# Kernel optimization log

Measured on AMD Instinct MI355X. Metric: run time of the kernel, lower is better.

## Reference

```python
import jax, jax.numpy as jnp
import numpy as np


def silu(x):
    return x * jax.nn.sigmoid(x)


def setup_inputs() -> dict:
    key = jax.random.key(0)
    B, L, Din = 2, 512, 128
    E, K = 2, 4
    d = E * Din          # inner dim = 256
    N = d                # state size forced to hid_dim = expansion*input_dim
    R = d // 16          # dt low-rank = 16
    ks = jax.random.split(key, 12)
    s = 0.02
    rn = lambda k, sh: (jax.random.normal(k, sh, jnp.float32) * s)
    return {
        "x":      jax.random.normal(ks[0], (B, L, Din), jnp.float32),
        "W_in":   rn(ks[1], (Din, d)),  "b_in":  jnp.zeros((d,), jnp.float32),
        "W_res":  rn(ks[2], (Din, d)),  "b_res": jnp.zeros((d,), jnp.float32),
        "conv_w": rn(ks[3], (d, d, K)), "conv_b": jnp.zeros((d,), jnp.float32),
        "W_xdt":  rn(ks[4], (d, R)),
        "W_dt":   rn(ks[5], (R, d)),
        "b_dt":   jnp.full((d,), -4.6, jnp.float32),  # softplus -> dt ~ 0.01
        "W_B":    rn(ks[6], (d, N)),
        "W_C":    rn(ks[7], (d, N)),
        "A_log":  jnp.log(jnp.broadcast_to(jnp.arange(1, N + 1, dtype=jnp.float32), (d, N))),
        "D":      jnp.ones((d,), jnp.float32),
        "W_out":  rn(ks[8], (d, Din)), "b_out": jnp.zeros((Din,), jnp.float32),
    }


def reference(x, W_in, b_in, W_res, b_res, conv_w, conv_b,
              W_xdt, W_dt, b_dt, W_B, W_C, A_log, D, W_out, b_out):
    k = conv_w.shape[-1]
    # input projections
    xi = x @ W_in + b_in               # [B,L,d]
    x_res = silu(x @ W_res + b_res)    # [B,L,d] gate branch
    # causal full (groups=1) conv1d: padding k-1, truncated to length L
    c = jax.lax.conv_general_dilated(
        xi.transpose(0, 2, 1), conv_w, window_strides=(1,),
        padding=[(k - 1, 0)], dimension_numbers=("NCH", "OIH", "NCH"))
    u = silu((c + conv_b[None, :, None]).transpose(0, 2, 1))  # [B,L,d]
    # S6 selective scan
    delta = jax.nn.softplus((u @ W_xdt) @ W_dt + b_dt)  # [B,L,d]
    Bm = u @ W_B                                        # [B,L,N]
    Cm = u @ W_C                                        # [B,L,N]
    A = -jnp.exp(A_log)                                 # [d,N]

    def step(h, xs):
        u_t, d_t, B_t, C_t = xs                         # [B,d],[B,d],[B,N],[B,N]
        dA = jnp.exp(d_t[:, :, None] * A)               # [B,d,N]
        h = dA * h + (d_t * u_t)[:, :, None] * B_t[:, None, :]
        y = jnp.einsum("bdn,bn->bd", h, C_t)
        return h, y

    h0 = jnp.zeros((x.shape[0], A.shape[0], A.shape[1]), xi.dtype)
    xs = (u.transpose(1, 0, 2), delta.transpose(1, 0, 2),
          Bm.transpose(1, 0, 2), Cm.transpose(1, 0, 2))
    _, ys = jax.lax.scan(step, h0, xs)                  # ys: [L,B,d]
    y = ys.transpose(1, 0, 2) + u * D                   # skip connection D*u
    # residual gate + output projection (norm disabled)
    return (y + x_res) @ W_out + b_out
```

## Files before the change

### kernel.cpp

```cpp
#include <hip/hip_runtime.h>
#include <hip/hip_bf16.h>

#define kB   2
#define kL   512
#define kBL  1024
#define kDin 128
#define kD   256
#define kN   256
#define kR   16
#define kK   4
#define kS   8
#define kT   64

__device__ __forceinline__ float silu_f(float v) { return v / (1.f + __expf(-v)); }
__device__ __forceinline__ float softplus_f(float z) {
    return (z > 20.f) ? z : log1pf(__expf(z));
}
__device__ __forceinline__ float4 f4fma(float s, float4 w, float4 a) {
    a.x += s * w.x; a.y += s * w.y; a.z += s * w.z; a.w += s * w.w; return a;
}

__global__ void __launch_bounds__(256) pre_kernel(
        const float* __restrict__ x, const float* __restrict__ W_in,
        const float* __restrict__ b_in, const float* __restrict__ W_res,
        const float* __restrict__ b_res, const float* __restrict__ conv_w,
        float* __restrict__ wT, float* __restrict__ xi, float* __restrict__ xres) {
    __shared__ float tile[32][33];
    __shared__ float xs[2][kDin];
    __shared__ float red[128][9];
    int bid = blockIdx.x, tid = threadIdx.x;
    if (bid < 256) {
        int c0 = (bid & 31) * 32, r0 = (bid >> 5) * 32;
        int tx = tid & 31, ty = tid >> 5;
        #pragma unroll
        for (int j = 0; j < 32; j += 8)
            tile[ty + j][tx] = conv_w[(r0 + ty + j) * 1024 + c0 + tx];
        __syncthreads();
        #pragma unroll
        for (int j = 0; j < 32; j += 8)
            wT[(c0 + ty + j) * 256 + r0 + tx] = tile[tx][ty + j];
        return;
    }
    int bt0 = (bid - 256) * 2;
    xs[tid >> 7][tid & 127] = x[bt0 * kDin + tid];
    __syncthreads();
    int q = tid & 63, m = (tid >> 6) & 1, ks = tid >> 7;
    const float* W = m ? W_res : W_in;
    float4 a0 = {0,0,0,0}, a1 = {0,0,0,0};
    int i0 = ks * 64;
    #pragma unroll 4
    for (int i = i0; i < i0 + 64; i++) {
        float4 w = ((const float4*)(W + i * kD))[q];
        a0 = f4fma(xs[0][i], w, a0);
        a1 = f4fma(xs[1][i], w, a1);
    }
    if (ks) {
        float* rr = red[tid - 128];
        rr[0] = a0.x; rr[1] = a0.y; rr[2] = a0.z; rr[3] = a0.w;
        rr[4] = a1.x; rr[5] = a1.y; rr[6] = a1.z; rr[7] = a1.w;
    }
    __syncthreads();
    if (!ks) {
        const float* rr = red[tid];
        a0.x += rr[0]; a0.y += rr[1]; a0.z += rr[2]; a0.w += rr[3];
        a1.x += rr[4]; a1.y += rr[5]; a1.z += rr[6]; a1.w += rr[7];
        float4 bv = ((const float4*)(m ? b_res : b_in))[q];
        a0.x += bv.x; a0.y += bv.y; a0.z += bv.z; a0.w += bv.w;
        a1.x += bv.x; a1.y += bv.y; a1.z += bv.z; a1.w += bv.w;
        if (m) {
            float4 s0 = {silu_f(a0.x), silu_f(a0.y), silu_f(a0.z), silu_f(a0.w)};
            float4 s1 = {silu_f(a1.x), silu_f(a1.y), silu_f(a1.z), silu_f(a1.w)};
            ((float4*)(xres + (bt0 + 0) * kD))[q] = s0;
            ((float4*)(xres + (bt0 + 1) * kD))[q] = s1;
        } else {
            ((float4*)(xi + (bt0 + 0) * kD))[q] = a0;
            ((float4*)(xi + (bt0 + 1) * kD))[q] = a1;
        }
    }
}

__global__ void __launch_bounds__(512) conv_fwd(
        const float* __restrict__ xi, const float* __restrict__ wT,
        const float* __restrict__ conv_b, float* __restrict__ u) {
    __shared__ float xs[7][kD];
    __shared__ float red[7][64][17];
    int bid = blockIdx.x, tid = threadIdx.x;
    int b = bid >> 7, t0 = (bid & 127) * 4;
    for (int idx = tid; idx < 7 * kD; idx += 512) {
        int j = idx >> 8, i = idx & 255;
        int t = t0 - 3 + j;
        xs[j][i] = (t >= 0) ? xi[(b * kL + t) * kD + i] : 0.f;
    }
    __syncthreads();
    int q = tid & 63, ks = tid >> 6;
    float4 a[4] = {{0,0,0,0},{0,0,0,0},{0,0,0,0},{0,0,0,0}};
    int ik0 = ks * 128;
    #pragma unroll 4
    for (int ik = ik0; ik < ik0 + 128; ik++) {
        float4 w = ((const float4*)(wT + ik * kD))[q];
        int ii = ik >> 2, k = ik & 3;
        #pragma unroll
        for (int r = 0; r < 4; r++) a[r] = f4fma(xs[k + r][ii], w, a[r]);
    }
    if (ks) {
        float* rr = red[ks - 1][q];
        #pragma unroll
        for (int r = 0; r < 4; r++) {
            rr[4*r+0] = a[r].x; rr[4*r+1] = a[r].y;
            rr[4*r+2] = a[r].z; rr[4*r+3] = a[r].w;
        }
    }
    __syncthreads();
    if (!ks) {
        #pragma unroll
        for (int p = 0; p < 7; p++) {
            const float* rr = red[p][q];
            #pragma unroll
            for (int r = 0; r < 4; r++) {
                a[r].x += rr[4*r+0]; a[r].y += rr[4*r+1];
                a[r].z += rr[4*r+2]; a[r].w += rr[4*r+3];
            }
        }
        float4 cb = ((const float4*)conv_b)[q];
        #pragma unroll
        for (int r = 0; r < 4; r++) {
            float4 v = {silu_f(a[r].x + cb.x), silu_f(a[r].y + cb.y),
                        silu_f(a[r].z + cb.z), silu_f(a[r].w + cb.w)};
            ((float4*)(u + (b * kL + t0 + r) * kD))[q] = v;
        }
    }
}

__global__ void __launch_bounds__(256) proj_bcd(
        const float* __restrict__ u, const float* __restrict__ W_xdt,
        const float* __restrict__ W_dt, const float* __restrict__ b_dt,
        const float* __restrict__ W_B, const float* __restrict__ W_C,
        float* __restrict__ delta, float* __restrict__ Bm, float* __restrict__ Cm) {
    __shared__ float us[2][kD];
    __shared__ float tpart[128];
    __shared__ float ts[2][kR];
    __shared__ float red[128][9];
    int bt0 = blockIdx.x * 2, tid = threadIdx.x;
    us[0][tid] = u[(bt0 + 0) * kD + tid];
    us[1][tid] = u[(bt0 + 1) * kD + tid];
    __syncthreads();
    if (tid < 128) {
        int r = tid >> 6, j = (tid >> 2) & 15, kq = tid & 3;
        float acc = 0.f;
        #pragma unroll 4
        for (int i = kq * 64; i < kq * 64 + 64; i++)
            acc += us[r][i] * W_xdt[i * kR + j];
        tpart[tid] = acc;
    }
    __syncthreads();
    if (tid < 32) {
        int r = tid >> 4, j = tid & 15;
        int base = r * 64 + j * 4;
        ts[r][j] = tpart[base] + tpart[base+1] + tpart[base+2] + tpart[base+3];
    }
    __syncthreads();
    int q = tid & 63, m = (tid >> 6) & 1, ks = tid >> 7;
    const float* W = m ? W_C : W_B;
    float4 a0 = {0,0,0,0}, a1 = {0,0,0,0};
    int i0 = ks * 128;
    #pragma unroll 4
    for (int i = i0; i < i0 + 128; i++) {
        float4 w = ((const float4*)(W + i * kN))[q];
        a0 = f4fma(us[0][i], w, a0);
        a1 = f4fma(us[1][i], w, a1);
    }
    if (ks) {
        float* rr = red[tid - 128];
        rr[0] = a0.x; rr[1] = a0.y; rr[2] = a0.z; rr[3] = a0.w;
        rr[4] = a1.x; rr[5] = a1.y; rr[6] = a1.z; rr[7] = a1.w;
    }
    __syncthreads();
    if (!ks) {
        const float* rr = red[tid];
        a0.x += rr[0]; a0.y += rr[1]; a0.z += rr[2]; a0.w += rr[3];
        a1.x += rr[4]; a1.y += rr[5]; a1.z += rr[6]; a1.w += rr[7];
        float* O = m ? Cm : Bm;
        ((float4*)(O + (bt0 + 0) * kN))[q] = a0;
        ((float4*)(O + (bt0 + 1) * kN))[q] = a1;
    }
    if (tid < 64) {
        float4 d0 = {0,0,0,0}, d1 = {0,0,0,0};
        #pragma unroll
        for (int j = 0; j < kR; j++) {
            float4 w = ((const float4*)(W_dt + j * kD))[tid];
            d0 = f4fma(ts[0][j], w, d0);
            d1 = f4fma(ts[1][j], w, d1);
        }
        float4 bd = ((const float4*)b_dt)[tid];
        float4 o0 = {softplus_f(d0.x + bd.x), softplus_f(d0.y + bd.y),
                     softplus_f(d0.z + bd.z), softplus_f(d0.w + bd.w)};
        float4 o1 = {softplus_f(d1.x + bd.x), softplus_f(d1.y + bd.y),
                     softplus_f(d1.z + bd.z), softplus_f(d1.w + bd.w)};
        ((float4*)(delta + (bt0 + 0) * kD))[tid] = o0;
        ((float4*)(delta + (bt0 + 1) * kD))[tid] = o1;
    }
}

__global__ void __launch_bounds__(1024) scan_fused(
        const float* __restrict__ delta, const float* __restrict__ u,
        const float* __restrict__ Bm, const float* __restrict__ Cm,
        const float* __restrict__ A_log, float* __restrict__ ys) {
    __shared__ float4 hp4[2][kS][64];
    __shared__ float dt_s[16][kT];
    __shared__ float du_s[16][kT];
    __shared__ float dsumS[2][kS];
    int w = threadIdx.x >> 6, lane = threadIdx.x & 63;
    int s = w & 7, dd = w >> 3;
    int b = blockIdx.x >> 7, dp = blockIdx.x & 127;
    int d = dp * 2 + dd;

    float4 al = ((const float4*)(A_log + d * kN))[lane];
    float A0 = -__expf(al.x), A1 = -__expf(al.y);
    float A2 = -__expf(al.z), A3 = -__expf(al.w);

    int gtu = (b * kL + s * kT + lane) * kD + d;
    float my_dt = delta[gtu];
    float my_du = my_dt * u[gtu];

    float dsum = my_dt;
    #pragma unroll
    for (int off = 32; off; off >>= 1) dsum += __shfl_xor(dsum, off, 64);

    dt_s[w][lane] = my_dt;
    du_s[w][lane] = my_du;

    const float4* Bp = (const float4*)(Bm + (b * kL + s * kT) * kN) + lane;
    const float4* Cp = (const float4*)(Cm + (b * kL + s * kT) * kN) + lane;
    __syncthreads();

    float h0 = 0, h1 = 0, h2 = 0, h3 = 0;
    for (int c = 0; c < kT; c += 4) {
        float4 dt4 = *(const float4*)&dt_s[w][c];
        float4 du4 = *(const float4*)&du_s[w][c];
        float4 Bb[4];
        #pragma unroll
        for (int j = 0; j < 4; j++) Bb[j] = Bp[(c + j) * (kN / 4)];
        float dts[4] = {dt4.x, dt4.y, dt4.z, dt4.w};
        float dus[4] = {du4.x, du4.y, du4.z, du4.w};
        float e[4][4];
        #pragma unroll
        for (int j = 0; j < 4; j++) {
            e[j][0] = __expf(dts[j] * A0);
            e[j][1] = __expf(dts[j] * A1);
            e[j][2] = __expf(dts[j] * A2);
            e[j][3] = __expf(dts[j] * A3);
        }
        #pragma unroll
        for (int j = 0; j < 4; j++) {
            h0 = e[j][0] * h0 + dus[j] * Bb[j].x;
            h1 = e[j][1] * h1 + dus[j] * Bb[j].y;
            h2 = e[j][2] * h2 + dus[j] * Bb[j].z;
            h3 = e[j][3] * h3 + dus[j] * Bb[j].w;
        }
    }
    hp4[dd][s][lane] = make_float4(h0, h1, h2, h3);
    if (lane == 0) dsumS[dd][s] = dsum;
    __syncthreads();

    h0 = h1 = h2 = h3 = 0;
    float P = 0.f;
    for (int j = s - 1; j >= 0; j--) {
        float4 hv = hp4[dd][j][lane];
        h0 += __expf(A0 * P) * hv.x;
        h1 += __expf(A1 * P) * hv.y;
        h2 += __expf(A2 * P) * hv.z;
        h3 += __expf(A3 * P) * hv.w;
        P += dsumS[dd][j];
    }

    float my_y = 0.f;
    for (int c = 0; c < kT; c += 4) {
        float4 dt4 = *(const float4*)&dt_s[w][c];
        float4 du4 = *(const float4*)&du_s[w][c];
        float4 Bb[4], Cc[4];
        #pragma unroll
        for (int j = 0; j < 4; j++) {
            Bb[j] = Bp[(c + j) * (kN / 4)];
            Cc[j] = Cp[(c + j) * (kN / 4)];
        }
        float dts[4] = {dt4.x, dt4.y, dt4.z, dt4.w};
        float dus[4] = {du4.x, du4.y, du4.z, du4.w};
        float e[4][4];
        #pragma unroll
        for (int j = 0; j < 4; j++) {
            e[j][0] = __expf(dts[j] * A0);
            e[j][1] = __expf(dts[j] * A1);
            e[j][2] = __expf(dts[j] * A2);
            e[j][3] = __expf(dts[j] * A3);
        }
        #pragma unroll
        for (int j = 0; j < 4; j++) {
            h0 = e[j][0] * h0 + dus[j] * Bb[j].x;
            h1 = e[j][1] * h1 + dus[j] * Bb[j].y;
            h2 = e[j][2] * h2 + dus[j] * Bb[j].z;
            h3 = e[j][3] * h3 + dus[j] * Bb[j].w;
            float y = h0 * Cc[j].x + h1 * Cc[j].y + h2 * Cc[j].z + h3 * Cc[j].w;
            #pragma unroll
            for (int off = 32; off; off >>= 1) y += __shfl_xor(y, off, 64);
            my_y = (lane == c + j) ? y : my_y;
        }
    }
    ys[(b * kL + s * kT + lane) * kD + d] = my_y;
}

__global__ void __launch_bounds__(256) out_proj(
        const float* __restrict__ ys, const float* __restrict__ u,
        const float* __restrict__ Dv, const float* __restrict__ xres,
        const float* __restrict__ W_out, const float* __restrict__ b_out,
        float* __restrict__ out) {
    __shared__ float vs[2][kD];
    __shared__ float red[224][9];
    int bt0 = blockIdx.x * 2, tid = threadIdx.x;
    for (int idx = tid; idx < 512; idx += 256) {
        int r = idx >> 8, i = idx & 255;
        int g = (bt0 + r) * kD + i;
        vs[r][i] = ys[g] + u[g] * Dv[i] + xres[g];
    }
    __syncthreads();
    int q = tid & 31, ks = tid >> 5;
    float4 a0 = {0,0,0,0}, a1 = {0,0,0,0};
    int i0 = ks * 32;
    #pragma unroll 4
    for (int i = i0; i < i0 + 32; i++) {
        float4 w = ((const float4*)(W_out + i * kDin))[q];
        a0 = f4fma(vs[0][i], w, a0);
        a1 = f4fma(vs[1][i], w, a1);
    }
    if (ks) {
        float* rr = red[tid - 32];
        rr[0] = a0.x; rr[1] = a0.y; rr[2] = a0.z; rr[3] = a0.w;
        rr[4] = a1.x; rr[5] = a1.y; rr[6] = a1.z; rr[7] = a1.w;
    }
    __syncthreads();
    if (!ks) {
        #pragma unroll
        for (int p = 0; p < 7; p++) {
            const float* rr = red[p * 32 + tid];
            a0.x += rr[0]; a0.y += rr[1]; a0.z += rr[2]; a0.w += rr[3];
            a1.x += rr[4]; a1.y += rr[5]; a1.z += rr[6]; a1.w += rr[7];
        }
        float4 bv = ((const float4*)b_out)[q];
        a0.x += bv.x; a0.y += bv.y; a0.z += bv.z; a0.w += bv.w;
        a1.x += bv.x; a1.y += bv.y; a1.z += bv.z; a1.w += bv.w;
        ((float4*)(out + (bt0 + 0) * kDin))[q] = a0;
        ((float4*)(out + (bt0 + 1) * kDin))[q] = a1;
    }
}

extern "C" void kernel_launch(void* const* d_in, const int* in_sizes, int n_in,
                              void* d_out, int out_size, void* d_ws, size_t ws_size,
                              hipStream_t stream) {
    const float* x      = (const float*)d_in[0];
    const float* W_in   = (const float*)d_in[1];
    const float* b_in   = (const float*)d_in[2];
    const float* W_res  = (const float*)d_in[3];
    const float* b_res  = (const float*)d_in[4];
    const float* conv_w = (const float*)d_in[5];
    const float* conv_b = (const float*)d_in[6];
    const float* W_xdt  = (const float*)d_in[7];
    const float* W_dt   = (const float*)d_in[8];
    const float* b_dt   = (const float*)d_in[9];
    const float* W_B    = (const float*)d_in[10];
    const float* W_C    = (const float*)d_in[11];
    const float* A_log  = (const float*)d_in[12];
    const float* Dv     = (const float*)d_in[13];
    const float* W_out  = (const float*)d_in[14];
    const float* b_out  = (const float*)d_in[15];

    float* ws    = (float*)d_ws;
    float* slot0 = ws;
    float* xres  = ws + 1 * 262144;
    float* slot2 = ws + 2 * 262144;
    float* u     = ws + 3 * 262144;
    float* yss   = ws + 4 * 262144;
    float* Cmat  = ws + 5 * 262144;

    float* xi    = slot0;
    float* delta = slot0;
    float* wT    = slot2;
    float* Bmat  = slot2;

    pre_kernel<<<768, 256, 0, stream>>>(x, W_in, b_in, W_res, b_res, conv_w,
                                        wT, xi, xres);
    conv_fwd<<<256, 512, 0, stream>>>(xi, wT, conv_b, u);
    proj_bcd<<<512, 256, 0, stream>>>(u, W_xdt, W_dt, b_dt, W_B, W_C,
                                      delta, Bmat, Cmat);
    scan_fused<<<kB * 128, 1024, 0, stream>>>(delta, u, Bmat, Cmat, A_log, yss);
    out_proj<<<512, 256, 0, stream>>>(yss, u, Dv, xres, W_out, b_out,
                                      (float*)d_out);
}
```

Baseline: 171.6 us.

## Restructure chunked scan: LDS transpose-reduce for y and skip redundant segment passes

The per-timestep 6-stage cross-lane shuffle reduction of y is replaced by a per-wave LDS scratch transpose. Each block of 16 timesteps is written to shared memory and reduced with a strided sum plus two shuffles. Segment 0 now computes y during its first pass and skips the second. The last segment skips the state-only first pass, and a redundant barrier is removed. This adds about 80KB of LDS scratch and a more divergent wave workload across segments.

```diff
diff --git a/kernel.cpp b/kernel.cpp
--- a/kernel.cpp
+++ b/kernel.cpp
@@ -209,6 +209,7 @@
     __shared__ float dt_s[16][kT];
     __shared__ float du_s[16][kT];
     __shared__ float dsumS[2][kS];
+    __shared__ float scr[16][64][20];
     int w = threadIdx.x >> 6, lane = threadIdx.x & 63;
     int s = w & 7, dd = w >> 3;
     int b = blockIdx.x >> 7, dp = blockIdx.x & 127;
@@ -231,79 +232,110 @@
 
     const float4* Bp = (const float4*)(Bm + (b * kL + s * kT) * kN) + lane;
     const float4* Cp = (const float4*)(Cm + (b * kL + s * kT) * kN) + lane;
-    __syncthreads();
 
     float h0 = 0, h1 = 0, h2 = 0, h3 = 0;
-    for (int c = 0; c < kT; c += 4) {
-        float4 dt4 = *(const float4*)&dt_s[w][c];
-        float4 du4 = *(const float4*)&du_s[w][c];
-        float4 Bb[4];
-        #pragma unroll
-        for (int j = 0; j < 4; j++) Bb[j] = Bp[(c + j) * (kN / 4)];
-        float dts[4] = {dt4.x, dt4.y, dt4.z, dt4.w};
-        float dus[4] = {du4.x, du4.y, du4.z, du4.w};
-        float e[4][4];
-        #pragma unroll
-        for (int j = 0; j < 4; j++) {
-            e[j][0] = __expf(dts[j] * A0);
-            e[j][1] = __expf(dts[j] * A1);
-            e[j][2] = __expf(dts[j] * A2);
-            e[j][3] = __expf(dts[j] * A3);
-        }
-        #pragma unroll
-        for (int j = 0; j < 4; j++) {
-            h0 = e[j][0] * h0 + dus[j] * Bb[j].x;
-            h1 = e[j][1] * h1 + dus[j] * Bb[j].y;
-            h2 = e[j][2] * h2 + dus[j] * Bb[j].z;
-            h3 = e[j][3] * h3 + dus[j] * Bb[j].w;
-        }
-    }
-    hp4[dd][s][lane] = make_float4(h0, h1, h2, h3);
+    float my_y = 0.f;
+    int tt = lane & 15, qq = lane >> 4;
+
+    auto scan_seg_y = [&]() {
+        #pragma unroll
+        for (int r = 0; r < 4; r++) {
+            float yp[16];
+            #pragma unroll
+            for (int c0 = 0; c0 < 16; c0 += 4) {
+                int c = r * 16 + c0;
+                float4 dt4 = *(const float4*)&dt_s[w][c];
+                float4 du4 = *(const float4*)&du_s[w][c];
+                float4 Bb[4], Cc[4];
+                #pragma unroll
+                for (int j = 0; j < 4; j++) {
+                    Bb[j] = Bp[(c + j) * (kN / 4)];
+                    Cc[j] = Cp[(c + j) * (kN / 4)];
+                }
+                float dts[4] = {dt4.x, dt4.y, dt4.z, dt4.w};
+                float dus[4] = {du4.x, du4.y, du4.z, du4.w};
+                float e[4][4];
+                #pragma unroll
+                for (int j = 0; j < 4; j++) {
+                    e[j][0] = __expf(dts[j] * A0);
+                    e[j][1] = __expf(dts[j] * A1);
+                    e[j][2] = __expf(dts[j] * A2);
+                    e[j][3] = __expf(dts[j] * A3);
+                }
+                #pragma unroll
+                for (int j = 0; j < 4; j++) {
+                    h0 = e[j][0] * h0 + dus[j] * Bb[j].x;
+                    h1 = e[j][1] * h1 + dus[j] * Bb[j].y;
+                    h2 = e[j][2] * h2 + dus[j] * Bb[j].z;
+                    h3 = e[j][3] * h3 + dus[j] * Bb[j].w;
+                    yp[c0 + j] = h0 * Cc[j].x + h1 * Cc[j].y
+                               + h2 * Cc[j].z + h3 * Cc[j].w;
+                }
+            }
+            float* mw = &scr[w][lane][0];
+            *(float4*)(mw + 0)  = make_float4(yp[0],  yp[1],  yp[2],  yp[3]);
+            *(float4*)(mw + 4)  = make_float4(yp[4],  yp[5],  yp[6],  yp[7]);
+            *(float4*)(mw + 8)  = make_float4(yp[8],  yp[9],  yp[10], yp[11]);
+            *(float4*)(mw + 12) = make_float4(yp[12], yp[13], yp[14], yp[15]);
+            float acc = 0.f;
+            #pragma unroll
+            for (int m = 0; m < 16; m++)
+                acc += scr[w][16 * qq + m][tt];
+            acc += __shfl_xor(acc, 16, 64);
+            acc += __shfl_xor(acc, 32, 64);
+            my_y = (qq == r) ? acc : my_y;
+        }
+    };
+    auto scan_seg = [&]() {
+        #pragma unroll 4
+        for (int c = 0; c < kT; c += 4) {
+            float4 dt4 = *(const float4*)&dt_s[w][c];
+            float4 du4 = *(const float4*)&du_s[w][c];
+            float4 Bb[4];
+            #pragma unroll
+            for (int j = 0; j < 4; j++) Bb[j] = Bp[(c + j) * (kN / 4)];
+            float dts[4] = {dt4.x, dt4.y, dt4.z, dt4.w};
+            float dus[4] = {du4.x, du4.y, du4.z, du4.w};
+            float e[4][4];
+            #pragma unroll
+            for (int j = 0; j < 4; j++) {
+                e[j][0] = __expf(dts[j] * A0);
+                e[j][1] = __expf(dts[j] * A1);
+                e[j][2] = __expf(dts[j] * A2);
+                e[j][3] = __expf(dts[j] * A3);
+            }
+            #pragma unroll
+            for (int j = 0; j < 4; j++) {
+                h0 = e[j][0] * h0 + dus[j] * Bb[j].x;
+                h1 = e[j][1] * h1 + dus[j] * Bb[j].y;
+                h2 = e[j][2] * h2 + dus[j] * Bb[j].z;
+                h3 = e[j][3] * h3 + dus[j] * Bb[j].w;
+            }
+        }
+    };
+
+    if (s == 0) {
+        scan_seg_y();
+        hp4[dd][0][lane] = make_float4(h0, h1, h2, h3);
+    } else if (s < 7) {
+        scan_seg();
+        hp4[dd][s][lane] = make_float4(h0, h1, h2, h3);
+    }
     if (lane == 0) dsumS[dd][s] = dsum;
     __syncthreads();
 
-    h0 = h1 = h2 = h3 = 0;
-    float P = 0.f;
-    for (int j = s - 1; j >= 0; j--) {
-        float4 hv = hp4[dd][j][lane];
-        h0 += __expf(A0 * P) * hv.x;
-        h1 += __expf(A1 * P) * hv.y;
-        h2 += __expf(A2 * P) * hv.z;
-        h3 += __expf(A3 * P) * hv.w;
-        P += dsumS[dd][j];
-    }
-
-    float my_y = 0.f;
-    for (int c = 0; c < kT; c += 4) {
-        float4 dt4 = *(const float4*)&dt_s[w][c];
-        float4 du4 = *(const float4*)&du_s[w][c];
-        float4 Bb[4], Cc[4];
-        #pragma unroll
-        for (int j = 0; j < 4; j++) {
-            Bb[j] = Bp[(c + j) * (kN / 4)];
-            Cc[j] = Cp[(c + j) * (kN / 4)];
-        }
-        float dts[4] = {dt4.x, dt4.y, dt4.z, dt4.w};
-        float dus[4] = {du4.x, du4.y, du4.z, du4.w};
-        float e[4][4];
-        #pragma unroll
-        for (int j = 0; j < 4; j++) {
-            e[j][0] = __expf(dts[j] * A0);
-            e[j][1] = __expf(dts[j] * A1);
-            e[j][2] = __expf(dts[j] * A2);
-            e[j][3] = __expf(dts[j] * A3);
-        }
-        #pragma unroll
-        for (int j = 0; j < 4; j++) {
-            h0 = e[j][0] * h0 + dus[j] * Bb[j].x;
-            h1 = e[j][1] * h1 + dus[j] * Bb[j].y;
-            h2 = e[j][2] * h2 + dus[j] * Bb[j].z;
-            h3 = e[j][3] * h3 + dus[j] * Bb[j].w;
-            float y = h0 * Cc[j].x + h1 * Cc[j].y + h2 * Cc[j].z + h3 * Cc[j].w;
-            #pragma unroll
-            for (int off = 32; off; off >>= 1) y += __shfl_xor(y, off, 64);
-            my_y = (lane == c + j) ? y : my_y;
-        }
+    if (s > 0) {
+        h0 = h1 = h2 = h3 = 0;
+        float P = 0.f;
+        for (int j = s - 1; j >= 0; j--) {
+            float4 hv = hp4[dd][j][lane];
+            h0 += __expf(A0 * P) * hv.x;
+            h1 += __expf(A1 * P) * hv.y;
+            h2 += __expf(A2 * P) * hv.z;
+            h3 += __expf(A3 * P) * hv.w;
+            P += dsumS[dd][j];
+        }
+        scan_seg_y();
     }
     ys[(b * kL + s * kT + lane) * kD + d] = my_y;
 }
```

Result: slower. 188.0 us (+9.5%).

## Skip redundant segment scans and use transpose-reduce for per-step outputs

Applied to the files above, without the earlier changes.

Segment 0 now computes its outputs directly in the first pass, since its initial state is zero, and the last segment skips the first-pass state scan because no later segment needs its carry. The per-timestep 64-lane butterfly reduction is replaced by a 4-way transpose exchange followed by a shared reduction over groups of four steps, which cuts shuffle count per step. It also adds an occupancy hint to launch bounds. The price is warp-level load imbalance between segments and more code paths in the kernel.

```diff
diff --git a/kernel.cpp b/kernel.cpp
--- a/kernel.cpp
+++ b/kernel.cpp
@@ -201,7 +201,7 @@
     }
 }
 
-__global__ void __launch_bounds__(1024) scan_fused(
+__global__ void __launch_bounds__(1024, 4) scan_fused(
         const float* __restrict__ delta, const float* __restrict__ u,
         const float* __restrict__ Bm, const float* __restrict__ Cm,
         const float* __restrict__ A_log, float* __restrict__ ys) {
@@ -234,76 +234,106 @@
     __syncthreads();
 
     float h0 = 0, h1 = 0, h2 = 0, h3 = 0;
-    for (int c = 0; c < kT; c += 4) {
-        float4 dt4 = *(const float4*)&dt_s[w][c];
-        float4 du4 = *(const float4*)&du_s[w][c];
-        float4 Bb[4];
-        #pragma unroll
-        for (int j = 0; j < 4; j++) Bb[j] = Bp[(c + j) * (kN / 4)];
-        float dts[4] = {dt4.x, dt4.y, dt4.z, dt4.w};
-        float dus[4] = {du4.x, du4.y, du4.z, du4.w};
-        float e[4][4];
-        #pragma unroll
-        for (int j = 0; j < 4; j++) {
-            e[j][0] = __expf(dts[j] * A0);
-            e[j][1] = __expf(dts[j] * A1);
-            e[j][2] = __expf(dts[j] * A2);
-            e[j][3] = __expf(dts[j] * A3);
-        }
-        #pragma unroll
-        for (int j = 0; j < 4; j++) {
-            h0 = e[j][0] * h0 + dus[j] * Bb[j].x;
-            h1 = e[j][1] * h1 + dus[j] * Bb[j].y;
-            h2 = e[j][2] * h2 + dus[j] * Bb[j].z;
-            h3 = e[j][3] * h3 + dus[j] * Bb[j].w;
-        }
-    }
-    hp4[dd][s][lane] = make_float4(h0, h1, h2, h3);
+    float my_y = 0.f;
+    int i1 = lane & 1, i2 = lane & 2;
+
+    auto scan_seg_y = [&]() {
+        for (int c = 0; c < kT; c += 4) {
+            float4 dt4 = *(const float4*)&dt_s[w][c];
+            float4 du4 = *(const float4*)&du_s[w][c];
+            float4 Bb[4], Cc[4];
+            #pragma unroll
+            for (int j = 0; j < 4; j++) {
+                Bb[j] = Bp[(c + j) * (kN / 4)];
+                Cc[j] = Cp[(c + j) * (kN / 4)];
+            }
+            float dts[4] = {dt4.x, dt4.y, dt4.z, dt4.w};
+            float dus[4] = {du4.x, du4.y, du4.z, du4.w};
+            float e[4][4];
+            #pragma unroll
+            for (int j = 0; j < 4; j++) {
+                e[j][0] = __expf(dts[j] * A0);
+                e[j][1] = __expf(dts[j] * A1);
+                e[j][2] = __expf(dts[j] * A2);
+                e[j][3] = __expf(dts[j] * A3);
+            }
+            float yp[4];
+            #pragma unroll
+            for (int j = 0; j < 4; j++) {
+                h0 = e[j][0] * h0 + dus[j] * Bb[j].x;
+                h1 = e[j][1] * h1 + dus[j] * Bb[j].y;
+                h2 = e[j][2] * h2 + dus[j] * Bb[j].z;
+                h3 = e[j][3] * h3 + dus[j] * Bb[j].w;
+                yp[j] = h0 * Cc[j].x + h1 * Cc[j].y + h2 * Cc[j].z + h3 * Cc[j].w;
+            }
+            float u0 = i1 ? yp[0] : yp[1];
+            float u1 = i1 ? yp[2] : yp[3];
+            float v0 = __shfl_xor(u0, 1, 64);
+            float v1 = __shfl_xor(u1, 1, 64);
+            if (i1) { yp[0] = v0; yp[2] = v1; } else { yp[1] = v0; yp[3] = v1; }
+            u0 = i2 ? yp[0] : yp[2];
+            u1 = i2 ? yp[1] : yp[3];
+            v0 = __shfl_xor(u0, 2, 64);
+            v1 = __shfl_xor(u1, 2, 64);
+            if (i2) { yp[0] = v0; yp[1] = v1; } else { yp[2] = v0; yp[3] = v1; }
+            float acc = (yp[0] + yp[1]) + (yp[2] + yp[3]);
+            acc += __shfl_xor(acc, 4, 64);
+            acc += __shfl_xor(acc, 8, 64);
+            acc += __shfl_xor(acc, 16, 64);
+            acc += __shfl_xor(acc, 32, 64);
+            my_y = ((lane >> 2) == (c >> 2)) ? acc : my_y;
+        }
+    };
+    auto scan_seg = [&]() {
+        #pragma unroll 4
+        for (int c = 0; c < kT; c += 4) {
+            float4 dt4 = *(const float4*)&dt_s[w][c];
+            float4 du4 = *(const float4*)&du_s[w][c];
+            float4 Bb[4];
+            #pragma unroll
+            for (int j = 0; j < 4; j++) Bb[j] = Bp[(c + j) * (kN / 4)];
+            float dts[4] = {dt4.x, dt4.y, dt4.z, dt4.w};
+            float dus[4] = {du4.x, du4.y, du4.z, du4.w};
+            float e[4][4];
+            #pragma unroll
+            for (int j = 0; j < 4; j++) {
+                e[j][0] = __expf(dts[j] * A0);
+                e[j][1] = __expf(dts[j] * A1);
+                e[j][2] = __expf(dts[j] * A2);
+                e[j][3] = __expf(dts[j] * A3);
+            }
+            #pragma unroll
+            for (int j = 0; j < 4; j++) {
+                h0 = e[j][0] * h0 + dus[j] * Bb[j].x;
+                h1 = e[j][1] * h1 + dus[j] * Bb[j].y;
+                h2 = e[j][2] * h2 + dus[j] * Bb[j].z;
+                h3 = e[j][3] * h3 + dus[j] * Bb[j].w;
+            }
+        }
+    };
+
+    if (s == 0) {
+        scan_seg_y();
+        hp4[dd][0][lane] = make_float4(h0, h1, h2, h3);
+    } else if (s < 7) {
+        scan_seg();
+        hp4[dd][s][lane] = make_float4(h0, h1, h2, h3);
+    }
     if (lane == 0) dsumS[dd][s] = dsum;
     __syncthreads();
 
-    h0 = h1 = h2 = h3 = 0;
-    float P = 0.f;
-    for (int j = s - 1; j >= 0; j--) {
-        float4 hv = hp4[dd][j][lane];
-        h0 += __expf(A0 * P) * hv.x;
-        h1 += __expf(A1 * P) * hv.y;
-        h2 += __expf(A2 * P) * hv.z;
-        h3 += __expf(A3 * P) * hv.w;
-        P += dsumS[dd][j];
-    }
-
-    float my_y = 0.f;
-    for (int c = 0; c < kT; c += 4) {
-        float4 dt4 = *(const float4*)&dt_s[w][c];
-        float4 du4 = *(const float4*)&du_s[w][c];
-        float4 Bb[4], Cc[4];
-        #pragma unroll
-        for (int j = 0; j < 4; j++) {
-            Bb[j] = Bp[(c + j) * (kN / 4)];
-            Cc[j] = Cp[(c + j) * (kN / 4)];
-        }
-        float dts[4] = {dt4.x, dt4.y, dt4.z, dt4.w};
-        float dus[4] = {du4.x, du4.y, du4.z, du4.w};
-        float e[4][4];
-        #pragma unroll
-        for (int j = 0; j < 4; j++) {
-            e[j][0] = __expf(dts[j] * A0);
-            e[j][1] = __expf(dts[j] * A1);
-            e[j][2] = __expf(dts[j] * A2);
-            e[j][3] = __expf(dts[j] * A3);
-        }
-        #pragma unroll
-        for (int j = 0; j < 4; j++) {
-            h0 = e[j][0] * h0 + dus[j] * Bb[j].x;
-            h1 = e[j][1] * h1 + dus[j] * Bb[j].y;
-            h2 = e[j][2] * h2 + dus[j] * Bb[j].z;
-            h3 = e[j][3] * h3 + dus[j] * Bb[j].w;
-            float y = h0 * Cc[j].x + h1 * Cc[j].y + h2 * Cc[j].z + h3 * Cc[j].w;
-            #pragma unroll
-            for (int off = 32; off; off >>= 1) y += __shfl_xor(y, off, 64);
-            my_y = (lane == c + j) ? y : my_y;
-        }
+    if (s > 0) {
+        h0 = h1 = h2 = h3 = 0;
+        float P = 0.f;
+        for (int j = s - 1; j >= 0; j--) {
+            float4 hv = hp4[dd][j][lane];
+            h0 += __expf(A0 * P) * hv.x;
+            h1 += __expf(A1 * P) * hv.y;
+            h2 += __expf(A2 * P) * hv.z;
+            h3 += __expf(A3 * P) * hv.w;
+            P += dsumS[dd][j];
+        }
+        scan_seg_y();
     }
     ys[(b * kL + s * kT + lane) * kD + d] = my_y;
 }
```

Result: no change. 172.6 us (+0.5%).
